# Performance work log

Hardware: AMD Instinct MI355X
Metric: run time of the kernel (lower is better)

## Reference

```python
import jax, jax.numpy as jnp
import numpy as np

N_NODES = 100000
N_EDGES = 1600000


def setup_inputs() -> dict:
    key = jax.random.key(0)
    k1, k2, k3, k4 = jax.random.split(key, 4)
    x = jax.random.normal(k1, (N_NODES, 128), dtype=jnp.float32)
    edge_index = jax.random.randint(k2, (2, N_EDGES), 0, N_NODES, dtype=jnp.int64)
    # Glorot-ish init for weights
    W1 = jax.random.normal(k3, (128, 128), dtype=jnp.float32) * (1.0 / np.sqrt(128))
    b1 = jnp.zeros((128,), dtype=jnp.float32)
    W2 = jax.random.normal(k4, (128, 64), dtype=jnp.float32) * (1.0 / np.sqrt(128))
    b2 = jnp.zeros((64,), dtype=jnp.float32)
    return {"x": x, "edge_index": edge_index, "W1": W1, "b1": b1, "W2": W2, "b2": b2}


def _gcn_conv(x, src, dst, W, b):
    """PyG GCNConv: h = W x; symmetric deg^-1/2 norm over edges (incl. self-loops); scatter-add; + bias."""
    n = x.shape[0]
    h = x @ W  # [N, out]
    ones = jnp.ones(src.shape[0], dtype=h.dtype)
    deg = jax.ops.segment_sum(ones, dst, num_segments=n)  # in-degree incl self-loops
    dinv = jax.lax.rsqrt(jnp.maximum(deg, 1e-12))
    norm = dinv[src] * dinv[dst]  # [E+N]
    msg = h[src] * norm[:, None]  # [E+N, out] gather
    out = jax.ops.segment_sum(msg, dst, num_segments=n)  # scatter-add
    return out + b


def reference(x, edge_index, W1, b1, W2, b2):
    n = x.shape[0]
    loop = jnp.arange(n, dtype=edge_index.dtype)
    src = jnp.concatenate([edge_index[0], loop])  # add self-loops
    dst = jnp.concatenate([edge_index[1], loop])
    h = jax.nn.relu(_gcn_conv(x, src, dst, W1, b1))
    # dropout is identity in eval mode
    return _gcn_conv(h, src, dst, W2, b2)
```

## Files before the change

kernel.cpp:

```cpp
#include <hip/hip_runtime.h>
#include <hip/hip_bf16.h>

#define THREADS 256
#define BSHIFT 9
#define BIN_CHUNK 4096
#define KP 136

typedef __attribute__((ext_vector_type(8))) short bf16x8;
typedef __attribute__((ext_vector_type(8))) unsigned short u16x8;
typedef __attribute__((ext_vector_type(4))) float f32x4;


__device__ inline unsigned short f2bf(float f) {
    unsigned int u = __float_as_uint(f);
    unsigned int r = (u + 0x7fffu + ((u >> 16) & 1u)) >> 16;
    return (unsigned short)r;
}

__device__ inline float2 bf2_to_f2(unsigned int u) {
    float2 r;
    r.x = __uint_as_float(u << 16);
    r.y = __uint_as_float(u & 0xffff0000u);
    return r;
}

__device__ inline void accum_row(float* acc, uint4 v) {
    float2 a = bf2_to_f2(v.x), b = bf2_to_f2(v.y), c = bf2_to_f2(v.z), d = bf2_to_f2(v.w);
    acc[0] += a.x; acc[1] += a.y; acc[2] += b.x; acc[3] += b.y;
    acc[4] += c.x; acc[5] += c.y; acc[6] += d.x; acc[7] += d.y;
}

__device__ inline void accum_row_scaled(float* acc, uint4 v, float s) {
    float2 a = bf2_to_f2(v.x), b = bf2_to_f2(v.y), c = bf2_to_f2(v.z), d = bf2_to_f2(v.w);
    acc[0] = fmaf(s, a.x, acc[0]); acc[1] = fmaf(s, a.y, acc[1]);
    acc[2] = fmaf(s, b.x, acc[2]); acc[3] = fmaf(s, b.y, acc[3]);
    acc[4] = fmaf(s, c.x, acc[4]); acc[5] = fmaf(s, c.y, acc[5]);
    acc[6] = fmaf(s, d.x, acc[6]); acc[7] = fmaf(s, d.y, acc[7]);
}

__device__ inline bf16x8 load_bfrag(const float* __restrict__ W, int ldn, int k0, int col) {
    bf16x8 b;
#pragma unroll
    for (int i = 0; i < 8; ++i) b[i] = (short)f2bf(W[(size_t)(k0 + i) * ldn + col]);
    return b;
}


__global__ __launch_bounds__(256) void k_bin_gemm1(const int* __restrict__ src,
                                                   const int* __restrict__ dst,
                                                   int* __restrict__ bcur,
                                                   unsigned int* __restrict__ binned,
                                                   int E, int NB, int cap,
                                                   const float* __restrict__ x,
                                                   const float* __restrict__ W1,
                                                   unsigned short* __restrict__ h,
                                                   int M, int nbin) {
    __shared__ __align__(16) short As[64 * KP];
    const int t = threadIdx.x;

    if ((int)blockIdx.x < nbin) {
        int* bcnt = (int*)As;
        int* bres = bcnt + 256;
        bcnt[t] = 0;
        __syncthreads();
        int base = blockIdx.x * BIN_CHUNK;
        int sv[16], dv[16];
#pragma unroll
        for (int i = 0; i < 4; ++i) {
            int e0 = base + (i * 256 + t) * 4;
            if (e0 + 3 < E) {
                int4 s4 = *(const int4*)(src + e0);
                int4 d4 = *(const int4*)(dst + e0);
                sv[4 * i + 0] = s4.x; sv[4 * i + 1] = s4.y;
                sv[4 * i + 2] = s4.z; sv[4 * i + 3] = s4.w;
                dv[4 * i + 0] = d4.x; dv[4 * i + 1] = d4.y;
                dv[4 * i + 2] = d4.z; dv[4 * i + 3] = d4.w;
            } else {
                for (int k = 0; k < 4; ++k) {
                    int e = e0 + k;
                    if (e < E) { sv[4 * i + k] = src[e]; dv[4 * i + k] = dst[e]; }
                    else dv[4 * i + k] = -1;
                }
            }
        }
#pragma unroll
        for (int i = 0; i < 16; ++i)
            if (dv[i] >= 0) atomicAdd(&bcnt[dv[i] >> BSHIFT], 1);
        __syncthreads();
        if (t < NB) {
            int old = bcnt[t] ? atomicAdd(&bcur[t], bcnt[t]) : 0;
            bres[t] = t * cap + old;
        }
        __syncthreads();
#pragma unroll
        for (int i = 0; i < 16; ++i) {
            if (dv[i] >= 0) {
                int b = dv[i] >> BSHIFT;
                int pos = atomicAdd(&bres[b], 1);
                if (pos < (b + 1) * cap)
                    binned[pos] = ((unsigned int)(dv[i] & 511) << 23) | (unsigned int)sv[i];
            }
        }
        return;
    }

    const int m0 = ((int)blockIdx.x - nbin) * 64;
    {
        int ar = t >> 5;
        int ac = (t & 31) * 4;
#pragma unroll
        for (int rb = 0; rb < 64; rb += 8) {
            int lrow = rb + ar;
            int row = m0 + lrow;
            ushort4 sv = make_ushort4(0, 0, 0, 0);
            if (row < M) {
                float4 v = *(const float4*)(x + (size_t)row * 128 + ac);
                sv.x = f2bf(v.x); sv.y = f2bf(v.y); sv.z = f2bf(v.z); sv.w = f2bf(v.w);
            }
            *(ushort4*)&As[lrow * KP + ac] = sv;
        }
    }
    __syncthreads();

    const int w = t >> 6;
    const int lane = t & 63;
    const int lm = lane & 15;
    const int qd = lane >> 4;
    const int n0w = w * 32;

    f32x4 acc[4][2];
#pragma unroll
    for (int mi = 0; mi < 4; ++mi)
#pragma unroll
        for (int ni = 0; ni < 2; ++ni) acc[mi][ni] = (f32x4){0.f, 0.f, 0.f, 0.f};

#pragma unroll
    for (int ks = 0; ks < 4; ++ks) {
        bf16x8 b0 = load_bfrag(W1, 128, ks * 32 + qd * 8, n0w + lm);
        bf16x8 b1 = load_bfrag(W1, 128, ks * 32 + qd * 8, n0w + 16 + lm);
#pragma unroll
        for (int mi = 0; mi < 4; ++mi) {
            bf16x8 a = *(const bf16x8*)&As[(mi * 16 + lm) * KP + ks * 32 + qd * 8];
            acc[mi][0] = __builtin_amdgcn_mfma_f32_16x16x32_bf16(a, b0, acc[mi][0], 0, 0, 0);
            acc[mi][1] = __builtin_amdgcn_mfma_f32_16x16x32_bf16(a, b1, acc[mi][1], 0, 0, 0);
        }
    }

#pragma unroll
    for (int mi = 0; mi < 4; ++mi) {
#pragma unroll
        for (int ni = 0; ni < 2; ++ni) {
            int col = n0w + ni * 16 + lm;
#pragma unroll
            for (int r = 0; r < 4; ++r) {
                int lrow = mi * 16 + qd * 4 + r;
                int row = m0 + lrow;
                if (row < M) h[(size_t)row * 128 + col] = f2bf(acc[mi][ni][r]);
            }
        }
    }
}

__global__ __launch_bounds__(256) void k_node_place(const unsigned int* __restrict__ binned,
                                                    const int* __restrict__ bcur, int cap,
                                                    int* __restrict__ rp,
                                                    int* __restrict__ deg,
                                                    float* __restrict__ dinv,
                                                    int* __restrict__ eperm, int N,
                                                    const float* __restrict__ W2,
                                                    unsigned short* __restrict__ W2t, int NB) {
    int b = blockIdx.x;
    int t = threadIdx.x;
    if (b == NB) {
        for (int i = t; i < 64 * 128; i += 256) {
            int nn = i >> 7;
            int kk = i & 127;
            W2t[i] = f2bf(W2[(size_t)kk * 64 + nn]);
        }
        return;
    }
    __shared__ int lc[512];
    __shared__ int s[256];
    int beg = b * cap;
    int end = beg + min(bcur[b], cap);
    int d0 = b << BSHIFT;
    lc[t] = 0;
    lc[t + 256] = 0;
    __syncthreads();
    for (int j = beg + t; j < end; j += 256) atomicAdd(&lc[binned[j] >> 23], 1);
    __syncthreads();
    int a = lc[2 * t], c = lc[2 * t + 1];
    int pair = a + c;
    s[t] = pair;
    __syncthreads();
    for (int off = 1; off < 256; off <<= 1) {
        int add = (t >= off) ? s[t - off] : 0;
        __syncthreads();
        s[t] += add;
        __syncthreads();
    }
    int excl = s[t] - pair;
    int st0 = beg + excl, st1 = st0 + a;
    int node0 = d0 + 2 * t;
    if (node0 < N) {
        rp[node0] = st0;
        deg[node0] = a;
        dinv[node0] = rsqrtf((float)a + 1.0f);
    }
    if (node0 + 1 < N) {
        rp[node0 + 1] = st1;
        deg[node0 + 1] = c;
        dinv[node0 + 1] = rsqrtf((float)c + 1.0f);
    }
    __syncthreads();
    lc[2 * t] = st0;
    lc[2 * t + 1] = st1;
    __syncthreads();
    for (int j = beg + t; j < end; j += 256) {
        unsigned int p = binned[j];
        int pos = atomicAdd(&lc[p >> 23], 1);
        eperm[pos] = (int)(p & 0x7fffffu);
    }
}


__global__ __launch_bounds__(256) void k_gather_gemm2(const int* __restrict__ rp,
                                                      const int* __restrict__ deg,
                                                      const int* __restrict__ eperm,
                                                      const float* __restrict__ dinv,
                                                      const uint4* __restrict__ h4,
                                                      const float* __restrict__ b1,
                                                      const unsigned short* __restrict__ W2t,
                                                      unsigned short* __restrict__ h2,
                                                      int n) {
    __shared__ __align__(16) short As[16 * KP];

    const int t = threadIdx.x;
    const int lane = t & 63;
    const int l16 = lane & 15;
    const int gbase = lane & 48;
    const int m0 = blockIdx.x * 16;
    const int lrow = (t >> 6) * 4 + (lane >> 4);
    const int node = m0 + lrow;
    const bool valid = node < n;

    int beg = 0, end = 0;
    float dv_self = 0.f;
    if (valid) {
        beg = rp[node];
        end = beg + deg[node];
        dv_self = dinv[node];
    }

    float acc[8];
#pragma unroll
    for (int i = 0; i < 8; ++i) acc[i] = 0.f;
    if (valid) accum_row_scaled(acc, h4[(size_t)node * 16 + l16], dv_self);

    for (int j = beg; j < end; j += 16) {
        int cnt = end - j;
        if (cnt > 16) cnt = 16;
        int ep = eperm[j + (l16 < cnt ? l16 : cnt - 1)];
        float dvv = dinv[ep];
        int k = 0;
        for (; k + 4 <= cnt; k += 4) {
            int i0 = __shfl(ep, gbase + k);
            int i1 = __shfl(ep, gbase + k + 1);
            int i2 = __shfl(ep, gbase + k + 2);
            int i3 = __shfl(ep, gbase + k + 3);
            float d0 = __shfl(dvv, gbase + k);
            float d1 = __shfl(dvv, gbase + k + 1);
            float d2 = __shfl(dvv, gbase + k + 2);
            float d3 = __shfl(dvv, gbase + k + 3);
            uint4 v0 = h4[(size_t)i0 * 16 + l16];
            uint4 v1 = h4[(size_t)i1 * 16 + l16];
            uint4 v2 = h4[(size_t)i2 * 16 + l16];
            uint4 v3 = h4[(size_t)i3 * 16 + l16];
            accum_row_scaled(acc, v0, d0);
            accum_row_scaled(acc, v1, d1);
            accum_row_scaled(acc, v2, d2);
            accum_row_scaled(acc, v3, d3);
        }
        for (; k < cnt; ++k) {
            int i0 = __shfl(ep, gbase + k);
            float d0 = __shfl(dvv, gbase + k);
            uint4 v0 = h4[(size_t)i0 * 16 + l16];
            accum_row_scaled(acc, v0, d0);
        }
    }

    {
        float4 bb0 = ((const float4*)b1)[l16 * 2];
        float4 bb1 = ((const float4*)b1)[l16 * 2 + 1];
        u16x8 s;
        s[0] = f2bf(fmaxf(fmaf(dv_self, acc[0], bb0.x), 0.f));
        s[1] = f2bf(fmaxf(fmaf(dv_self, acc[1], bb0.y), 0.f));
        s[2] = f2bf(fmaxf(fmaf(dv_self, acc[2], bb0.z), 0.f));
        s[3] = f2bf(fmaxf(fmaf(dv_self, acc[3], bb0.w), 0.f));
        s[4] = f2bf(fmaxf(fmaf(dv_self, acc[4], bb1.x), 0.f));
        s[5] = f2bf(fmaxf(fmaf(dv_self, acc[5], bb1.y), 0.f));
        s[6] = f2bf(fmaxf(fmaf(dv_self, acc[6], bb1.z), 0.f));
        s[7] = f2bf(fmaxf(fmaf(dv_self, acc[7], bb1.w), 0.f));
        *(u16x8*)&As[lrow * KP + l16 * 8] = s;
    }
    __syncthreads();

    const int w = t >> 6;
    const int lm = lane & 15;
    const int qd = lane >> 4;
    const int col = w * 16 + lm;

    f32x4 c4 = (f32x4){0.f, 0.f, 0.f, 0.f};
#pragma unroll
    for (int ks = 0; ks < 4; ++ks) {
        bf16x8 b = *(const bf16x8*)&W2t[(size_t)col * 128 + ks * 32 + qd * 8];
        bf16x8 a = *(const bf16x8*)&As[lm * KP + ks * 32 + qd * 8];
        c4 = __builtin_amdgcn_mfma_f32_16x16x32_bf16(a, b, c4, 0, 0, 0);
    }

#pragma unroll
    for (int r = 0; r < 4; ++r) {
        int row = m0 + qd * 4 + r;
        if (row < n) h2[(size_t)row * 64 + col] = f2bf(dinv[row] * c4[r]);
    }
}

__global__ __launch_bounds__(256) void k_gather64(const int* __restrict__ rp,
                                                  const int* __restrict__ deg,
                                                  const int* __restrict__ eperm,
                                                  const float* __restrict__ dinv,
                                                  const uint4* __restrict__ h4,
                                                  const float* __restrict__ bias,
                                                  float* __restrict__ out, int n) {
    const int t = threadIdx.x;
    const int lane = t & 63;
    const int l8 = lane & 7;
    const int gbase = lane & 56;
    const int node = blockIdx.x * 32 + (t >> 6) * 8 + (lane >> 3);
    const bool valid = node < n;

    int beg = 0, end = 0;
    if (valid) {
        beg = rp[node];
        end = beg + deg[node];
    }

    float acc[8];
#pragma unroll
    for (int i = 0; i < 8; ++i) acc[i] = 0.f;
    if (valid) accum_row(acc, h4[(size_t)node * 8 + l8]);

    int j = beg;
    for (; j + 16 <= end; j += 16) {
        int ep0 = eperm[j + l8];
        int ep1 = eperm[j + 8 + l8];
        int idx[16];
#pragma unroll
        for (int k = 0; k < 8; ++k) idx[k] = __shfl(ep0, gbase + k);
#pragma unroll
        for (int k = 0; k < 8; ++k) idx[8 + k] = __shfl(ep1, gbase + k);
        uint4 v[16];
#pragma unroll
        for (int k = 0; k < 16; ++k) v[k] = h4[(size_t)idx[k] * 8 + l8];
#pragma unroll
        for (int k = 0; k < 16; ++k) accum_row(acc, v[k]);
    }
    int cnt = end - j;
    if (cnt >= 8) {
        int ep = eperm[j + l8];
        int idx[8];
#pragma unroll
        for (int k = 0; k < 8; ++k) idx[k] = __shfl(ep, gbase + k);
        uint4 v[8];
#pragma unroll
        for (int k = 0; k < 8; ++k) v[k] = h4[(size_t)idx[k] * 8 + l8];
#pragma unroll
        for (int k = 0; k < 8; ++k) accum_row(acc, v[k]);
        j += 8;
        cnt -= 8;
    }
    if (cnt > 0) {
        int ep = eperm[j + (l8 < cnt ? l8 : cnt - 1)];
        int k = 0;
        for (; k + 4 <= cnt; k += 4) {
            int i0 = __shfl(ep, gbase + k);
            int i1 = __shfl(ep, gbase + k + 1);
            int i2 = __shfl(ep, gbase + k + 2);
            int i3 = __shfl(ep, gbase + k + 3);
            uint4 v0 = h4[(size_t)i0 * 8 + l8];
            uint4 v1 = h4[(size_t)i1 * 8 + l8];
            uint4 v2 = h4[(size_t)i2 * 8 + l8];
            uint4 v3 = h4[(size_t)i3 * 8 + l8];
            accum_row(acc, v0);
            accum_row(acc, v1);
            accum_row(acc, v2);
            accum_row(acc, v3);
        }
        for (; k < cnt; ++k) {
            int i0 = __shfl(ep, gbase + k);
            uint4 v0 = h4[(size_t)i0 * 8 + l8];
            accum_row(acc, v0);
        }
    }

    if (valid) {
        float dv = dinv[node];
        float4 b0 = ((const float4*)bias)[l8 * 2];
        float4 b1 = ((const float4*)bias)[l8 * 2 + 1];
        float4 o0, o1;
        o0.x = dv * acc[0] + b0.x; o0.y = dv * acc[1] + b0.y;
        o0.z = dv * acc[2] + b0.z; o0.w = dv * acc[3] + b0.w;
        o1.x = dv * acc[4] + b1.x; o1.y = dv * acc[5] + b1.y;
        o1.z = dv * acc[6] + b1.z; o1.w = dv * acc[7] + b1.w;
        float4* orow = (float4*)(out + (size_t)node * 64);
        orow[l8 * 2] = o0;
        orow[l8 * 2 + 1] = o1;
    }
}


extern "C" void kernel_launch(void* const* d_in, const int* in_sizes, int n_in,
                              void* d_out, int out_size, void* d_ws, size_t ws_size,
                              hipStream_t stream) {
    const float* x  = (const float*)d_in[0];
    const int*   ei = (const int*)d_in[1];
    const float* W1 = (const float*)d_in[2];
    const float* b1 = (const float*)d_in[3];
    const float* W2 = (const float*)d_in[4];
    const float* b2 = (const float*)d_in[5];
    float* out = (float*)d_out;

    const int N = in_sizes[0] / 128;
    const int E = in_sizes[1] / 2;
    const int* src = ei;
    const int* dst = ei + E;
    const int NB = (N + 511) >> BSHIFT;
    const int cap = (E + NB - 1) / NB + ((E / NB) >> 2) + 1024;

    char* ws = (char*)d_ws;
    size_t off = 0;
    auto carve = [&](size_t bytes) -> void* {
        void* p = ws + off;
        off = (off + bytes + 255) & ~(size_t)255;
        return p;
    };
    float* dinv = (float*)carve((size_t)N * 4);
    int*   rp   = (int*)carve((size_t)N * 4);
    int*   deg  = (int*)carve((size_t)N * 4);
    int*   bcur = (int*)carve(256 * 4);
    unsigned int* binned = (unsigned int*)carve((size_t)NB * cap * 4);
    int*   eperm = (int*)carve((size_t)NB * cap * 4);
    unsigned short* h   = (unsigned short*)carve((size_t)N * 128 * 2);
    unsigned short* h2  = (unsigned short*)carve((size_t)N * 64 * 2);
    unsigned short* W2t = (unsigned short*)carve(64 * 128 * 2);

    const int gMm = (N + 63) / 64;
    const int nbin = (E + BIN_CHUNK - 1) / BIN_CHUNK;

    hipMemsetAsync(bcur, 0, 256 * sizeof(int), stream);
    k_bin_gemm1<<<nbin + gMm, THREADS, 0, stream>>>(src, dst, bcur, binned, E, NB, cap,
                                                    x, W1, h, N, nbin);
    k_node_place<<<NB + 1, THREADS, 0, stream>>>(binned, bcur, cap, rp, deg, dinv, eperm, N,
                                                 W2, W2t, NB);

    k_gather_gemm2<<<(N + 15) / 16, THREADS, 0, stream>>>(rp, deg, eperm, dinv, (const uint4*)h,
                                                          b1, W2t, h2, N);

    k_gather64<<<(N + 31) / 32, THREADS, 0, stream>>>(rp, deg, eperm, dinv, (const uint4*)h2, b2, out, N);
}
```

Baseline: 256.6 us.

## Widen node_place to 512 threads; let last-finishing wave do GEMM2 tile

k_node_place now launches 512 threads per bin block, so the LDS histogram and scatter loops run with twice the threads while the scan stays on the first 256. In k_gather_gemm2 the block-wide barrier before the MFMA stage is replaced by a shared atomic counter, and only the last wave to finish its gather computes all four 16-column output tiles. This lets the other waves exit early instead of waiting at the barrier, at the cost of serializing the small GEMM onto one wave. Using __threadfence_block plus an atomic as the only ordering between waves' LDS writes and the final wave's reads is a fragile substitute for a barrier.

```diff
diff --git a/kernel.cpp b/kernel.cpp
--- a/kernel.cpp
+++ b/kernel.cpp
@@ -161,7 +161,7 @@
     }
 }
 
-__global__ __launch_bounds__(256) void k_node_place(const unsigned int* __restrict__ binned,
+__global__ __launch_bounds__(512) void k_node_place(const unsigned int* __restrict__ binned,
                                                     const int* __restrict__ bcur, int cap,
                                                     int* __restrict__ rp,
                                                     int* __restrict__ deg,
@@ -172,7 +172,7 @@
     int b = blockIdx.x;
     int t = threadIdx.x;
     if (b == NB) {
-        for (int i = t; i < 64 * 128; i += 256) {
+        for (int i = t; i < 64 * 128; i += 512) {
             int nn = i >> 7;
             int kk = i & 127;
             W2t[i] = f2bf(W2[(size_t)kk * 64 + nn]);
@@ -185,38 +185,47 @@
     int end = beg + min(bcur[b], cap);
     int d0 = b << BSHIFT;
     lc[t] = 0;
-    lc[t + 256] = 0;
-    __syncthreads();
-    for (int j = beg + t; j < end; j += 256) atomicAdd(&lc[binned[j] >> 23], 1);
-    __syncthreads();
-    int a = lc[2 * t], c = lc[2 * t + 1];
-    int pair = a + c;
-    s[t] = pair;
+    __syncthreads();
+    for (int j = beg + t; j < end; j += 512) atomicAdd(&lc[binned[j] >> 23], 1);
+    __syncthreads();
+    int a = 0, c = 0, pair = 0;
+    if (t < 256) {
+        a = lc[2 * t];
+        c = lc[2 * t + 1];
+        pair = a + c;
+        s[t] = pair;
+    }
     __syncthreads();
     for (int off = 1; off < 256; off <<= 1) {
-        int add = (t >= off) ? s[t - off] : 0;
+        int add = (t >= off && t < 256) ? s[t - off] : 0;
         __syncthreads();
-        s[t] += add;
+        if (t < 256) s[t] += add;
         __syncthreads();
     }
-    int excl = s[t] - pair;
-    int st0 = beg + excl, st1 = st0 + a;
-    int node0 = d0 + 2 * t;
-    if (node0 < N) {
-        rp[node0] = st0;
-        deg[node0] = a;
-        dinv[node0] = rsqrtf((float)a + 1.0f);
-    }
-    if (node0 + 1 < N) {
-        rp[node0 + 1] = st1;
-        deg[node0 + 1] = c;
-        dinv[node0 + 1] = rsqrtf((float)c + 1.0f);
-    }
-    __syncthreads();
-    lc[2 * t] = st0;
-    lc[2 * t + 1] = st1;
-    __syncthreads();
-    for (int j = beg + t; j < end; j += 256) {
+    int st0 = 0, st1 = 0;
+    if (t < 256) {
+        int excl = s[t] - pair;
+        st0 = beg + excl;
+        st1 = st0 + a;
+        int node0 = d0 + 2 * t;
+        if (node0 < N) {
+            rp[node0] = st0;
+            deg[node0] = a;
+            dinv[node0] = rsqrtf((float)a + 1.0f);
+        }
+        if (node0 + 1 < N) {
+            rp[node0 + 1] = st1;
+            deg[node0 + 1] = c;
+            dinv[node0 + 1] = rsqrtf((float)c + 1.0f);
+        }
+    }
+    __syncthreads();
+    if (t < 256) {
+        lc[2 * t] = st0;
+        lc[2 * t + 1] = st1;
+    }
+    __syncthreads();
+    for (int j = beg + t; j < end; j += 512) {
         unsigned int p = binned[j];
         int pos = atomicAdd(&lc[p >> 23], 1);
         eperm[pos] = (int)(p & 0x7fffffu);
@@ -234,6 +243,7 @@
                                                       unsigned short* __restrict__ h2,
                                                       int n) {
     __shared__ __align__(16) short As[16 * KP];
+    __shared__ int done;
 
     const int t = threadIdx.x;
     const int lane = t & 63;
@@ -243,6 +253,9 @@
     const int lrow = (t >> 6) * 4 + (lane >> 4);
     const int node = m0 + lrow;
     const bool valid = node < n;
+
+    if (t == 0) done = 0;
+    __syncthreads();
 
     int beg = 0, end = 0;
     float dv_self = 0.f;
@@ -303,25 +316,30 @@
         s[7] = f2bf(fmaxf(fmaf(dv_self, acc[7], bb1.w), 0.f));
         *(u16x8*)&As[lrow * KP + l16 * 8] = s;
     }
-    __syncthreads();
-
-    const int w = t >> 6;
+
+    __threadfence_block();
+    int lastv = 0;
+    if (lane == 0) lastv = (atomicAdd(&done, 1) == 3) ? 1 : 0;
+    lastv = __shfl(lastv, 0);
+    if (!lastv) return;
+
     const int lm = lane & 15;
     const int qd = lane >> 4;
-    const int col = w * 16 + lm;
-
-    f32x4 c4 = (f32x4){0.f, 0.f, 0.f, 0.f};
-#pragma unroll
-    for (int ks = 0; ks < 4; ++ks) {
-        bf16x8 b = *(const bf16x8*)&W2t[(size_t)col * 128 + ks * 32 + qd * 8];
-        bf16x8 a = *(const bf16x8*)&As[lm * KP + ks * 32 + qd * 8];
-        c4 = __builtin_amdgcn_mfma_f32_16x16x32_bf16(a, b, c4, 0, 0, 0);
-    }
-
-#pragma unroll
-    for (int r = 0; r < 4; ++r) {
-        int row = m0 + qd * 4 + r;
-        if (row < n) h2[(size_t)row * 64 + col] = f2bf(dinv[row] * c4[r]);
+#pragma unroll
+    for (int wt = 0; wt < 4; ++wt) {
+        const int col = wt * 16 + lm;
+        f32x4 c4 = (f32x4){0.f, 0.f, 0.f, 0.f};
+#pragma unroll
+        for (int ks = 0; ks < 4; ++ks) {
+            bf16x8 b = *(const bf16x8*)&W2t[(size_t)col * 128 + ks * 32 + qd * 8];
+            bf16x8 a = *(const bf16x8*)&As[lm * KP + ks * 32 + qd * 8];
+            c4 = __builtin_amdgcn_mfma_f32_16x16x32_bf16(a, b, c4, 0, 0, 0);
+        }
+#pragma unroll
+        for (int r = 0; r < 4; ++r) {
+            int row = m0 + qd * 4 + r;
+            if (row < n) h2[(size_t)row * 64 + col] = f2bf(dinv[row] * c4[r]);
+        }
     }
 }
 
@@ -460,8 +478,8 @@
     hipMemsetAsync(bcur, 0, 256 * sizeof(int), stream);
     k_bin_gemm1<<<nbin + gMm, THREADS, 0, stream>>>(src, dst, bcur, binned, E, NB, cap,
                                                     x, W1, h, N, nbin);
-    k_node_place<<<NB + 1, THREADS, 0, stream>>>(binned, bcur, cap, rp, deg, dinv, eperm, N,
-                                                 W2, W2t, NB);
+    k_node_place<<<NB + 1, 512, 0, stream>>>(binned, bcur, cap, rp, deg, dinv, eperm, N,
+                                             W2, W2t, NB);
 
     k_gather_gemm2<<<(N + 15) / 16, THREADS, 0, stream>>>(rp, deg, eperm, dinv, (const uint4*)h,
                                                           b1, W2t, h2, N);
```

Result: faster. 248.9 us (-3.0%).
